# Optimization experiments

Measured on AMD Instinct MI355X. Metric: run time of the kernel, lower is better.

The kernel has to match this reference:

```python
import jax, jax.numpy as jnp
import numpy as np

VOCAB, D_MODEL, N_STATE, H_HEADS, LAYERS = 64, 512, 32, 16, 4
EXPAND = 2
D_INNER = EXPAND * D_MODEL          # 1024
P_HEAD = D_INNER // H_HEADS         # 64
CONV_DIM = D_INNER + 2 * N_STATE    # x, B, C share the depthwise conv
K_CONV = 4
D_IN_PROJ = 2 * D_INNER + 2 * N_STATE + H_HEADS  # z, x, B, C, dt
BATCH, SEQ = 4, 1024
EPS = 1e-5


def rmsnorm(x, w):
    return x * jax.lax.rsqrt(jnp.mean(x * x, axis=-1, keepdims=True) + EPS) * w


def silu(x):
    return x * jax.nn.sigmoid(x)


def causal_depthwise_conv(x, w, b):
    # x: [B,L,C], w: [C,K], b: [C]; causal (left) padding, depthwise groups
    xt = jnp.transpose(x, (0, 2, 1))  # [B,C,L]
    out = jax.lax.conv_general_dilated(xt, w[:, None, :], (1,), [(K_CONV - 1, 0)], feature_group_count=w.shape[0])
    return jnp.transpose(out, (0, 2, 1)) + b


def ssd(xh, dt, A, Bm, Cm, Dp):
    # Mamba2 SSD recurrence. xh [B,L,H,P], dt [B,L,H], A [H], Bm/Cm [B,L,N], Dp [H]
    dA = jnp.exp(dt * A)              # decay per (batch, step, head)
    dtx = dt[..., None] * xh          # [B,L,H,P]

    def step(h, inp):
        dA_t, dtx_t, B_t, C_t = inp
        # h: [B,H,P,N]
        h = dA_t[:, :, None, None] * h + dtx_t[..., None] * B_t[:, None, None, :]
        y = jnp.einsum('bhpn,bn->bhp', h, C_t)
        return h, y

    h0 = jnp.zeros((xh.shape[0], H_HEADS, P_HEAD, N_STATE), xh.dtype)
    _, ys = jax.lax.scan(step, h0, (jnp.moveaxis(dA, 1, 0), jnp.moveaxis(dtx, 1, 0), jnp.moveaxis(Bm, 1, 0), jnp.moveaxis(Cm, 1, 0)))
    return jnp.moveaxis(ys, 0, 1) + xh * Dp[None, None, :, None]


def mamba_block(x, norm_w, W_in, b_in, conv_w, conv_b, dt_bias, A_log, Dp, gnorm_w, W_out, b_out):
    res = x
    u = rmsnorm(x, norm_w)
    zxbcdt = u @ W_in + b_in                                # [B,L,D_IN_PROJ]
    z = zxbcdt[..., :D_INNER]
    xBC = zxbcdt[..., D_INNER:D_INNER + CONV_DIM]
    dt = zxbcdt[..., D_INNER + CONV_DIM:]                   # [B,L,H]
    xBC = silu(causal_depthwise_conv(xBC, conv_w, conv_b))
    xc = xBC[..., :D_INNER]
    Bm = xBC[..., D_INNER:D_INNER + N_STATE]
    Cm = xBC[..., D_INNER + N_STATE:]
    dt = jax.nn.softplus(dt + dt_bias)
    xh = xc.reshape(xc.shape[0], xc.shape[1], H_HEADS, P_HEAD)
    y = ssd(xh, dt, -jnp.exp(A_log), Bm, Cm, Dp)
    y = y.reshape(y.shape[0], y.shape[1], D_INNER)
    y = rmsnorm(y * silu(z), gnorm_w)                       # gated RMSNorm
    return res + y @ W_out + b_out


def forward(input_tokens, emb, norm_w, W_in, b_in, conv_w, conv_b, dt_bias, A_log, D_param, gnorm_w, W_out, b_out, head_w, head_b):
    h = emb[input_tokens]
    for i in range(LAYERS):
        h = mamba_block(h, norm_w[i], W_in[i], b_in[i], conv_w[i], conv_b[i], dt_bias[i], A_log[i], D_param[i], gnorm_w[i], W_out[i], b_out[i])
    return h @ head_w + head_b


def setup_inputs() -> dict:
    key = jax.random.key(0)
    ks = jax.random.split(key, 8)
    s = 0.02
    return {
        'input_tokens': jax.random.randint(ks[0], (BATCH, SEQ), 0, VOCAB),
        'emb': jax.random.normal(ks[1], (VOCAB, D_MODEL), jnp.float32) * s,
        'norm_w': jnp.ones((LAYERS, D_MODEL), jnp.float32),
        'W_in': jax.random.normal(ks[2], (LAYERS, D_MODEL, D_IN_PROJ), jnp.float32) * s,
        'b_in': jnp.zeros((LAYERS, D_IN_PROJ), jnp.float32),
        'conv_w': jax.random.normal(ks[3], (LAYERS, CONV_DIM, K_CONV), jnp.float32) * 0.1,
        'conv_b': jnp.zeros((LAYERS, CONV_DIM), jnp.float32),
        'dt_bias': jnp.tile(jnp.log(jnp.expm1(jnp.linspace(0.001, 0.1, H_HEADS, dtype=jnp.float32))), (LAYERS, 1)),
        'A_log': jnp.tile(jnp.log(jnp.arange(1, H_HEADS + 1, dtype=jnp.float32)), (LAYERS, 1)),
        'D_param': jnp.ones((LAYERS, H_HEADS), jnp.float32),
        'gnorm_w': jnp.ones((LAYERS, D_INNER), jnp.float32),
        'W_out': jax.random.normal(ks[4], (LAYERS, D_INNER, D_MODEL), jnp.float32) * s,
        'b_out': jnp.zeros((LAYERS, D_MODEL), jnp.float32),
        'head_w': jax.random.normal(ks[5], (D_MODEL, VOCAB), jnp.float32) * s,
        'head_b': jnp.zeros((VOCAB,), jnp.float32),
    }


def reference(input_tokens, emb, norm_w, W_in, b_in, conv_w, conv_b, dt_bias, A_log, D_param, gnorm_w, W_out, b_out, head_w, head_b):
    return forward(input_tokens, emb, norm_w, W_in, b_in, conv_w, conv_b, dt_bias, A_log, D_param, gnorm_w, W_out, b_out, head_w, head_b)
```

## Files before the change

### kernel.cpp

```cpp
#include <hip/hip_runtime.h>
#include <hip/hip_bf16.h>

#define VOCAB     64
#define D_MODEL   512
#define N_STATE   32
#define H_HEADS   16
#define LAYERS    4
#define D_INNER   1024
#define P_HEAD    64
#define CONV_DIM  1088
#define K_CONV    4
#define D_IN_PROJ 2128
#define NPAD_IN   2176
#define NPAD_HEAD 128
#define BATCH     4
#define SEQ       1024
#define NTOK      (BATCH*SEQ)
#define EPS       1e-5f
#define CL        64
#define NC        (SEQ/CL)
#define PSTR      80

typedef __bf16 bf16x8 __attribute__((ext_vector_type(8)));
typedef float  f32x4  __attribute__((ext_vector_type(4)));

__device__ __forceinline__ float sigmoidf_(float x) { return 1.f / (1.f + __expf(-x)); }
__device__ __forceinline__ float softplusf_(float x) { return (x > 20.f) ? x : log1pf(__expf(x)); }

__global__ void embed_kernel(const int* __restrict__ tok, const float* __restrict__ emb,
                             float* __restrict__ h) {
  int idx = blockIdx.x * 256 + threadIdx.x;
  if (idx >= NTOK * D_MODEL) return;
  int d = idx & (D_MODEL - 1);
  int t = idx >> 9;
  h[idx] = emb[tok[t] * D_MODEL + d];
}

__global__ void rmsnorm512_kernel(const float* __restrict__ x, const float* __restrict__ w,
                                  __bf16* __restrict__ out) {
  int tok = blockIdx.x;
  int tid = threadIdx.x;
  const float* xr = x + (size_t)tok * D_MODEL;
  float v0 = xr[tid], v1 = xr[tid + 256];
  float ss = v0 * v0 + v1 * v1;
  #pragma unroll
  for (int o = 32; o >= 1; o >>= 1) ss += __shfl_xor(ss, o);
  __shared__ float red[4];
  if ((tid & 63) == 0) red[tid >> 6] = ss;
  __syncthreads();
  float tot = red[0] + red[1] + red[2] + red[3];
  float sc = rsqrtf(tot * (1.f / D_MODEL) + EPS);
  out[(size_t)tok * D_MODEL + tid]       = (__bf16)(v0 * sc * w[tid]);
  out[(size_t)tok * D_MODEL + tid + 256] = (__bf16)(v1 * sc * w[tid + 256]);
}

__global__ void transpose_cast_kernel(const float* __restrict__ W, __bf16* __restrict__ Wt,
                                      int K, int N, int Npad) {
  W  += (size_t)blockIdx.z * K * N;
  Wt += (size_t)blockIdx.z * Npad * K;
  __shared__ float T[32][33];
  int n0 = blockIdx.x * 32, k0 = blockIdx.y * 32;
  int tx = threadIdx.x & 31, ty = threadIdx.x >> 5;
  #pragma unroll
  for (int i = 0; i < 4; i++) {
    int n = n0 + tx;
    T[ty + i * 8][tx] = (n < N) ? W[(size_t)(k0 + ty + i * 8) * N + n] : 0.f;
  }
  __syncthreads();
  #pragma unroll
  for (int i = 0; i < 4; i++)
    Wt[(size_t)(n0 + ty + i * 8) * K + k0 + tx] = (__bf16)T[tx][ty + i * 8];
}

#define TM 64
#define TN 128
#define TK 64
__global__ __launch_bounds__(256) void gemm_bf16_kernel(
    const __bf16* __restrict__ A, const __bf16* __restrict__ Bt,
    const float* __restrict__ bias, const float* __restrict__ res,
    float* __restrict__ C, __bf16* __restrict__ Cbf, int K, int N, int ldc) {
  __shared__ __bf16 As[TM * TK];
  __shared__ __bf16 Bs[TN * TK];
  int tid = threadIdx.x;
  int lane = tid & 63, wave = tid >> 6;
  int wm = wave >> 1, wn = wave & 1;
  int q = lane >> 4, l16 = lane & 15;
  size_t row0 = (size_t)blockIdx.y * TM;
  int col0 = blockIdx.x * TN;
  const __bf16* Ab = A + row0 * K;
  const __bf16* Bb = Bt + (size_t)col0 * K;

  bf16x8 pa[2], pb[4];
  #pragma unroll
  for (int r = 0; r < 2; r++) {
    int lin = r * 256 + tid;
    pa[r] = *(const bf16x8*)(Ab + (size_t)(lin >> 3) * K + (lin & 7) * 8);
  }
  #pragma unroll
  for (int r = 0; r < 4; r++) {
    int lin = r * 256 + tid;
    pb[r] = *(const bf16x8*)(Bb + (size_t)(lin >> 3) * K + (lin & 7) * 8);
  }

  f32x4 acc[2][4];
  #pragma unroll
  for (int i = 0; i < 2; i++)
    #pragma unroll
    for (int j = 0; j < 4; j++) acc[i][j] = (f32x4){0.f, 0.f, 0.f, 0.f};

  for (int k0 = 0; k0 < K; k0 += TK) {
    #pragma unroll
    for (int r = 0; r < 2; r++) { int lin = r * 256 + tid; *(bf16x8*)(As + lin * 8) = pa[r]; }
    #pragma unroll
    for (int r = 0; r < 4; r++) { int lin = r * 256 + tid; *(bf16x8*)(Bs + lin * 8) = pb[r]; }
    __syncthreads();
    int kn = k0 + TK;
    if (kn < K) {
      #pragma unroll
      for (int r = 0; r < 2; r++) {
        int lin = r * 256 + tid;
        pa[r] = *(const bf16x8*)(Ab + (size_t)(lin >> 3) * K + kn + (lin & 7) * 8);
      }
      #pragma unroll
      for (int r = 0; r < 4; r++) {
        int lin = r * 256 + tid;
        pb[r] = *(const bf16x8*)(Bb + (size_t)(lin >> 3) * K + kn + (lin & 7) * 8);
      }
    }
    #pragma unroll
    for (int ks = 0; ks < 2; ks++) {
      bf16x8 af[2], bfv[4];
      #pragma unroll
      for (int i = 0; i < 2; i++)
        af[i] = *(const bf16x8*)(As + (wm * 32 + i * 16 + l16) * TK + ks * 32 + q * 8);
      #pragma unroll
      for (int j = 0; j < 4; j++)
        bfv[j] = *(const bf16x8*)(Bs + (wn * 64 + j * 16 + l16) * TK + ks * 32 + q * 8);
      #pragma unroll
      for (int i = 0; i < 2; i++)
        #pragma unroll
        for (int j = 0; j < 4; j++)
          acc[i][j] = __builtin_amdgcn_mfma_f32_16x16x32_bf16(af[i], bfv[j], acc[i][j], 0, 0, 0);
    }
    __syncthreads();
  }

  #pragma unroll
  for (int i = 0; i < 2; i++) {
    size_t mrow = row0 + wm * 32 + i * 16 + q * 4;
    #pragma unroll
    for (int j = 0; j < 4; j++) {
      int col = col0 + wn * 64 + j * 16 + l16;
      if (col < N) {
        float bv = bias ? bias[col] : 0.f;
        #pragma unroll
        for (int rr = 0; rr < 4; rr++) {
          size_t off = (mrow + rr) * (size_t)ldc + col;
          float v = acc[i][j][rr] + bv;
          if (res) v += res[off];
          if (C)   C[off] = v;
          if (Cbf) Cbf[off] = (__bf16)v;
        }
      }
    }
  }
}

__device__ __forceinline__ void wave0_dt_cumsum(
    const __bf16* __restrict__ zxbf, const float* __restrict__ dt_bias,
    int b, int h, int t0, int tid, float* ldt, float* lcs) {
  if (tid < 64) {
    float dv = (float)zxbf[((size_t)(b * SEQ + t0 + tid)) * D_IN_PROJ + 2 * D_INNER + 2 * N_STATE + h]
               + dt_bias[h];
    float dtv = softplusf_(dv);
    float cs = dtv;
    #pragma unroll
    for (int off = 1; off < 64; off <<= 1) {
      float o = __shfl_up(cs, off);
      if (tid >= off) cs += o;
    }
    ldt[tid] = dtv;
    lcs[tid] = cs;
  }
}

__global__ __launch_bounds__(256) void ssd_local_kernel(
    const __bf16* __restrict__ zxbf, const float* __restrict__ conv_w,
    const float* __restrict__ conv_b, const float* __restrict__ dt_bias,
    const float* __restrict__ A_log,
    float* __restrict__ Slocal, float* __restrict__ dAprod) {
  int blk = blockIdx.x;
  int c = blk % NC;
  int h = (blk / NC) % H_HEADS;
  int b = blk / (NC * H_HEADS);
  int tid = threadIdx.x;
  int lane = tid & 63, wave = tid >> 6;
  int q = lane >> 4, l16 = lane & 15;
  int t0 = c * CL;
  float A = -__expf(A_log[h]);
  __shared__ __bf16 rawx[68][64];
  __shared__ __bf16 rawB[68][32];
  __shared__ __bf16 lxT[64][PSTR];
  __shared__ __bf16 lBT[32][PSTR];
  __shared__ float ldt[64], lcs[64];
  for (int i = tid; i < 68 * 8; i += 256) {
    int r = i >> 3, c0 = (i & 7) * 8;
    int gr = t0 - 3 + r;
    bf16x8 v;
    #pragma unroll
    for (int k = 0; k < 8; k++) v[k] = (__bf16)0.f;
    if (gr >= 0)
      v = *(const bf16x8*)(zxbf + ((size_t)(b * SEQ + gr)) * D_IN_PROJ + D_INNER + h * 64 + c0);
    *(bf16x8*)(&rawx[r][c0]) = v;
  }
  for (int i = tid; i < 68 * 4; i += 256) {
    int r = i >> 2, c0 = (i & 3) * 8;
    int gr = t0 - 3 + r;
    bf16x8 v;
    #pragma unroll
    for (int k = 0; k < 8; k++) v[k] = (__bf16)0.f;
    if (gr >= 0)
      v = *(const bf16x8*)(zxbf + ((size_t)(b * SEQ + gr)) * D_IN_PROJ + 2 * D_INNER + c0);
    *(bf16x8*)(&rawB[r][c0]) = v;
  }
  wave0_dt_cumsum(zxbf, dt_bias, b, h, t0, tid, ldt, lcs);
  __syncthreads();
  float cs63 = lcs[63];
  {
    int p = tid & 63;
    const float* w = conv_w + (h * 64 + p) * K_CONV;
    float w0 = w[0], w1 = w[1], w2 = w[2], w3 = w[3];
    float cb = conv_b[h * 64 + p];
    for (int i = tid; i < CL * 64; i += 256) {
      int t = i >> 6;
      float a = cb + w0 * (float)rawx[t][p] + w1 * (float)rawx[t + 1][p]
                   + w2 * (float)rawx[t + 2][p] + w3 * (float)rawx[t + 3][p];
      lxT[p][t] = (__bf16)(a * sigmoidf_(a));
    }
  }
  {
    int n = tid & 31;
    const float* w = conv_w + (D_INNER + n) * K_CONV;
    float w0 = w[0], w1 = w[1], w2 = w[2], w3 = w[3];
    float cb = conv_b[D_INNER + n];
    for (int i = tid; i < CL * 32; i += 256) {
      int t = i >> 5;
      float a = cb + w0 * (float)rawB[t][n] + w1 * (float)rawB[t + 1][n]
                   + w2 * (float)rawB[t + 2][n] + w3 * (float)rawB[t + 3][n];
      float v = a * sigmoidf_(a);
      float wt = ldt[t] * __expf(A * (cs63 - lcs[t]));
      lBT[n][t] = (__bf16)(v * wt);
    }
  }
  __syncthreads();
  f32x4 acc[2];
  acc[0] = (f32x4){0.f,0.f,0.f,0.f}; acc[1] = (f32x4){0.f,0.f,0.f,0.f};
  #pragma unroll
  for (int kb = 0; kb < 2; kb++) {
    bf16x8 af = *(const bf16x8*)(&lxT[wave * 16 + l16][kb * 32 + q * 8]);
    #pragma unroll
    for (int j = 0; j < 2; j++) {
      bf16x8 bf = *(const bf16x8*)(&lBT[l16 + 16 * j][kb * 32 + q * 8]);
      acc[j] = __builtin_amdgcn_mfma_f32_16x16x32_bf16(af, bf, acc[j], 0, 0, 0);
    }
  }
  float* dst = Slocal + (size_t)blk * 2048;
  #pragma unroll
  for (int j = 0; j < 2; j++) {
    int n = l16 + 16 * j;
    #pragma unroll
    for (int rr = 0; rr < 4; rr++) {
      int p = wave * 16 + q * 4 + rr;
      dst[p * 32 + n] = acc[j][rr];
    }
  }
  if (tid == 0) dAprod[blk] = __expf(A * cs63);
}

__global__ void ssd_combine_kernel(float* __restrict__ S, const float* __restrict__ dAprod) {
  int bh = blockIdx.x;
  int e = threadIdx.x * 8;
  float st[8] = {};
  for (int c = 0; c < NC; c++) {
    float* ptr = S + ((size_t)(bh * NC + c)) * 2048 + e;
    float pr = dAprod[bh * NC + c];
    float tmp[8];
    #pragma unroll
    for (int j = 0; j < 8; j++) tmp[j] = ptr[j];
    #pragma unroll
    for (int j = 0; j < 8; j++) { ptr[j] = st[j]; st[j] = pr * st[j] + tmp[j]; }
  }
}

__global__ __launch_bounds__(256) void ssd_out_kernel(
    const __bf16* __restrict__ zxbf, const float* __restrict__ conv_w,
    const float* __restrict__ conv_b, const float* __restrict__ dt_bias,
    const float* __restrict__ A_log, const float* __restrict__ Dp,
    const float* __restrict__ Sstart, __bf16* __restrict__ y) {
  int blk = blockIdx.x;
  int c = blk % NC;
  int h = (blk / NC) % H_HEADS;
  int b = blk / (NC * H_HEADS);
  int tid = threadIdx.x;
  int lane = tid & 63, wave = tid >> 6;
  int q = lane >> 4, l16 = lane & 15;
  int t0 = c * CL;
  float A = -__expf(A_log[h]);
  float D = Dp[h];
  __shared__ __bf16 rawbuf[2 * 68 * 64];
  __shared__ __bf16 lxT[64][PSTR];
  __shared__ __bf16 lB[64][32];
  __shared__ __bf16 lC[64][32];
  __shared__ __bf16 lS[64][32];
  __shared__ float ldt[64], lcs[64];
  __bf16* rawx = rawbuf;
  __bf16* rawBC = rawbuf + 68 * 64;
  for (int i = tid; i < 68 * 8; i += 256) {
    int r = i >> 3, c0 = (i & 7) * 8;
    int gr = t0 - 3 + r;
    bf16x8 vx, vbc;
    #pragma unroll
    for (int k = 0; k < 8; k++) { vx[k] = (__bf16)0.f; vbc[k] = (__bf16)0.f; }
    if (gr >= 0) {
      const __bf16* rowp = zxbf + ((size_t)(b * SEQ + gr)) * D_IN_PROJ;
      vx  = *(const bf16x8*)(rowp + D_INNER + h * 64 + c0);
      vbc = *(const bf16x8*)(rowp + 2 * D_INNER + c0);
    }
    *(bf16x8*)(rawx + r * 64 + c0)  = vx;
    *(bf16x8*)(rawBC + r * 64 + c0) = vbc;
  }
  wave0_dt_cumsum(zxbf, dt_bias, b, h, t0, tid, ldt, lcs);
  __syncthreads();
  {
    int p = tid & 63;
    const float* w = conv_w + (h * 64 + p) * K_CONV;
    float w0 = w[0], w1 = w[1], w2 = w[2], w3 = w[3];
    float cb = conv_b[h * 64 + p];
    for (int i = tid; i < CL * 64; i += 256) {
      int t = i >> 6;
      float a = cb + w0 * (float)rawx[t * 64 + p] + w1 * (float)rawx[(t + 1) * 64 + p]
                   + w2 * (float)rawx[(t + 2) * 64 + p] + w3 * (float)rawx[(t + 3) * 64 + p];
      lxT[p][t] = (__bf16)(a * sigmoidf_(a));
    }
  }
  {
    int col = tid & 63;
    const float* w = conv_w + (D_INNER + col) * K_CONV;
    float w0 = w[0], w1 = w[1], w2 = w[2], w3 = w[3];
    float cb = conv_b[D_INNER + col];
    for (int i = tid; i < CL * 64; i += 256) {
      int t = i >> 6;
      float a = cb + w0 * (float)rawBC[t * 64 + col] + w1 * (float)rawBC[(t + 1) * 64 + col]
                   + w2 * (float)rawBC[(t + 2) * 64 + col] + w3 * (float)rawBC[(t + 3) * 64 + col];
      float v = a * sigmoidf_(a);
      if (col < 32) lB[t][col] = (__bf16)v; else lC[t][col - 32] = (__bf16)v;
    }
  }
  {
    const float* src = Sstart + (size_t)blk * 2048;
    for (int i = tid; i < 2048; i += 256) lS[i >> 5][i & 31] = (__bf16)src[i];
  }
  __syncthreads();
  bf16x8 afC = *(const bf16x8*)(&lC[wave * 16 + l16][q * 8]);
  f32x4 accG[4], accI[4], accY[4];
  #pragma unroll
  for (int j = 0; j < 4; j++) {
    accG[j] = (f32x4){0.f,0.f,0.f,0.f};
    accI[j] = (f32x4){0.f,0.f,0.f,0.f};
    accY[j] = (f32x4){0.f,0.f,0.f,0.f};
  }
  #pragma unroll
  for (int j = 0; j < 4; j++) {
    bf16x8 bf = *(const bf16x8*)(&lB[l16 + 16 * j][q * 8]);
    accG[j] = __builtin_amdgcn_mfma_f32_16x16x32_bf16(afC, bf, accG[j], 0, 0, 0);
  }
  #pragma unroll
  for (int j = 0; j < 4; j++) {
    bf16x8 bf = *(const bf16x8*)(&lS[l16 + 16 * j][q * 8]);
    accI[j] = __builtin_amdgcn_mfma_f32_16x16x32_bf16(afC, bf, accI[j], 0, 0, 0);
  }
  __bf16* pP = rawbuf + wave * 16 * PSTR;
  #pragma unroll
  for (int j = 0; j < 4; j++) {
    int s = l16 + 16 * j;
    float css = lcs[s], dts = ldt[s];
    #pragma unroll
    for (int rr = 0; rr < 4; rr++) {
      int tl = q * 4 + rr;
      int t = wave * 16 + tl;
      float val = accG[j][rr] * __expf(A * (lcs[t] - css)) * dts;
      if (s == t) val += D;
      if (s > t) val = 0.f;
      pP[tl * PSTR + s] = (__bf16)val;
    }
  }
  #pragma unroll
  for (int kb = 0; kb < 2; kb++) {
    bf16x8 afP = *(const bf16x8*)(pP + l16 * PSTR + kb * 32 + q * 8);
    #pragma unroll
    for (int j = 0; j < 4; j++) {
      bf16x8 bf = *(const bf16x8*)(&lxT[l16 + 16 * j][kb * 32 + q * 8]);
      accY[j] = __builtin_amdgcn_mfma_f32_16x16x32_bf16(afP, bf, accY[j], 0, 0, 0);
    }
  }
  #pragma unroll
  for (int rr = 0; rr < 4; rr++) {
    int t = wave * 16 + q * 4 + rr;
    float cumt = __expf(A * lcs[t]);
    __bf16* yrow = y + ((size_t)(b * SEQ + t0 + t)) * D_INNER + h * 64;
    #pragma unroll
    for (int j = 0; j < 4; j++) {
      int p = l16 + 16 * j;
      yrow[p] = (__bf16)(accY[j][rr] + cumt * accI[j][rr]);
    }
  }
}

__global__ void gate_norm_kernel(const __bf16* __restrict__ zxbf, const float* __restrict__ gw,
                                 const __bf16* __restrict__ y, __bf16* __restrict__ ybf) {
  int tok = blockIdx.x;
  int tid = threadIdx.x;
  const __bf16* zr = zxbf + (size_t)tok * D_IN_PROJ;
  const __bf16* yr = y + (size_t)tok * D_INNER;
  float v[4];
  float ss = 0.f;
  #pragma unroll
  for (int i = 0; i < 4; i++) {
    int d = tid + i * 256;
    float z = (float)zr[d];
    float g = (float)yr[d] * z * sigmoidf_(z);
    v[i] = g;
    ss += g * g;
  }
  #pragma unroll
  for (int o = 32; o >= 1; o >>= 1) ss += __shfl_xor(ss, o);
  __shared__ float red[4];
  if ((tid & 63) == 0) red[tid >> 6] = ss;
  __syncthreads();
  float tot = red[0] + red[1] + red[2] + red[3];
  float sc = rsqrtf(tot * (1.f / D_INNER) + EPS);
  #pragma unroll
  for (int i = 0; i < 4; i++) {
    int d = tid + i * 256;
    ybf[(size_t)tok * D_INNER + d] = (__bf16)(v[i] * sc * gw[d]);
  }
}

extern "C" void kernel_launch(void* const* d_in, const int* in_sizes, int n_in,
                              void* d_out, int out_size, void* d_ws, size_t ws_size,
                              hipStream_t stream) {
  const int*   tok     = (const int*)  d_in[0];
  const float* emb     = (const float*)d_in[1];
  const float* norm_w  = (const float*)d_in[2];
  const float* W_in    = (const float*)d_in[3];
  const float* b_in    = (const float*)d_in[4];
  const float* conv_w  = (const float*)d_in[5];
  const float* conv_b  = (const float*)d_in[6];
  const float* dt_bias = (const float*)d_in[7];
  const float* A_log   = (const float*)d_in[8];
  const float* D_par   = (const float*)d_in[9];
  const float* gnorm_w = (const float*)d_in[10];
  const float* W_out   = (const float*)d_in[11];
  const float* b_out   = (const float*)d_in[12];
  const float* head_w  = (const float*)d_in[13];
  const float* head_b  = (const float*)d_in[14];
  float* out = (float*)d_out;

  char* p = (char*)d_ws;
  auto alloc = [&](size_t bytes) { void* r = (void*)p; p += (bytes + 255) & ~(size_t)255; return r; };
  float*  h      = (float*) alloc((size_t)NTOK * D_MODEL * 4);
  float*  slocal = (float*) alloc((size_t)BATCH * H_HEADS * NC * P_HEAD * N_STATE * 4);
  float*  daprod = (float*) alloc((size_t)BATCH * H_HEADS * NC * 4);
  __bf16* y      = (__bf16*)alloc((size_t)NTOK * D_INNER * 2);
  __bf16* zxbf   = (__bf16*)alloc((size_t)NTOK * D_IN_PROJ * 2);
  __bf16* ubf    = (__bf16*)alloc((size_t)NTOK * D_MODEL * 2);
  __bf16* ybf    = (__bf16*)alloc((size_t)NTOK * D_INNER * 2);
  __bf16* hbf    = (__bf16*)alloc((size_t)NTOK * D_MODEL * 2);
  __bf16* WtIn   = (__bf16*)alloc((size_t)LAYERS * NPAD_IN * D_MODEL * 2);
  __bf16* WtOut  = (__bf16*)alloc((size_t)LAYERS * D_MODEL * D_INNER * 2);
  __bf16* WtHead = (__bf16*)alloc((size_t)NPAD_HEAD * D_MODEL * 2);

  transpose_cast_kernel<<<dim3(NPAD_IN / 32, D_MODEL / 32, LAYERS), 256, 0, stream>>>(
      W_in, WtIn, D_MODEL, D_IN_PROJ, NPAD_IN);
  transpose_cast_kernel<<<dim3(D_MODEL / 32, D_INNER / 32, LAYERS), 256, 0, stream>>>(
      W_out, WtOut, D_INNER, D_MODEL, D_MODEL);
  transpose_cast_kernel<<<dim3(NPAD_HEAD / 32, D_MODEL / 32, 1), 256, 0, stream>>>(
      head_w, WtHead, D_MODEL, VOCAB, NPAD_HEAD);

  embed_kernel<<<(NTOK * D_MODEL + 255) / 256, 256, 0, stream>>>(tok, emb, h);

  for (int l = 0; l < LAYERS; l++) {
    rmsnorm512_kernel<<<NTOK, 256, 0, stream>>>(h, norm_w + (size_t)l * D_MODEL, ubf);

    gemm_bf16_kernel<<<dim3(NPAD_IN / TN, NTOK / TM), 256, 0, stream>>>(
        ubf, WtIn + (size_t)l * NPAD_IN * D_MODEL, b_in + (size_t)l * D_IN_PROJ,
        nullptr, nullptr, zxbf, D_MODEL, D_IN_PROJ, D_IN_PROJ);

    ssd_local_kernel<<<BATCH * H_HEADS * NC, 256, 0, stream>>>(
        zxbf, conv_w + (size_t)l * CONV_DIM * K_CONV, conv_b + (size_t)l * CONV_DIM,
        dt_bias + (size_t)l * H_HEADS, A_log + (size_t)l * H_HEADS, slocal, daprod);
    ssd_combine_kernel<<<BATCH * H_HEADS, 256, 0, stream>>>(slocal, daprod);
    ssd_out_kernel<<<BATCH * H_HEADS * NC, 256, 0, stream>>>(
        zxbf, conv_w + (size_t)l * CONV_DIM * K_CONV, conv_b + (size_t)l * CONV_DIM,
        dt_bias + (size_t)l * H_HEADS, A_log + (size_t)l * H_HEADS,
        D_par + (size_t)l * H_HEADS, slocal, y);

    gate_norm_kernel<<<NTOK, 256, 0, stream>>>(zxbf, gnorm_w + (size_t)l * D_INNER, y, ybf);

    gemm_bf16_kernel<<<dim3(D_MODEL / TN, NTOK / TM), 256, 0, stream>>>(
        ybf, WtOut + (size_t)l * D_MODEL * D_INNER, b_out + (size_t)l * D_MODEL, h, h,
        (l == LAYERS - 1) ? hbf : nullptr, D_INNER, D_MODEL, D_MODEL);
  }

  gemm_bf16_kernel<<<dim3(NPAD_HEAD / TN, NTOK / TM), 256, 0, stream>>>(
      hbf, WtHead, head_b, nullptr, out, nullptr, D_MODEL, VOCAB, VOCAB);
}
```

Before: 497.6 us.

## Add 128x128 register-prefetched GEMM for in-projection and parallelize chunk-state combine

Adds a dedicated GEMM kernel with 128x128 output tiles per block, 4x4 MFMA accumulators per wave and register prefetch of the next K-slice, used for the input projection. This raises operand reuse per LDS load and overlaps global loads with MFMA work. Separately, the chunk-state combine kernel now splits each (batch, head) across two blocks, caches the decay factors in shared memory, and loads all chunk states up front as float4 vectors before the serial scan. The larger tile roughly halves the grid and raises register pressure, which can lower occupancy.

```diff
diff --git a/kernel.cpp b/kernel.cpp
--- a/kernel.cpp
+++ b/kernel.cpp
@@ -161,6 +161,86 @@
           if (C)   C[off] = v;
           if (Cbf) Cbf[off] = (__bf16)v;
         }
+      }
+    }
+  }
+}
+
+__global__ __launch_bounds__(256) void gemm_bf16_128(
+    const __bf16* __restrict__ A, const __bf16* __restrict__ Bt,
+    const float* __restrict__ bias, __bf16* __restrict__ Cbf,
+    int K, int N, int ldc) {
+  __shared__ __bf16 As[128 * TK];
+  __shared__ __bf16 Bs[128 * TK];
+  int tid = threadIdx.x;
+  int lane = tid & 63, wave = tid >> 6;
+  int wm = wave >> 1, wn = wave & 1;
+  int q = lane >> 4, l16 = lane & 15;
+  size_t row0 = (size_t)blockIdx.y * 128;
+  int col0 = blockIdx.x * 128;
+  const __bf16* Ab = A + row0 * K;
+  const __bf16* Bb = Bt + (size_t)col0 * K;
+
+  bf16x8 pa[4], pb[4];
+  #pragma unroll
+  for (int r = 0; r < 4; r++) {
+    int lin = r * 256 + tid;
+    pa[r] = *(const bf16x8*)(Ab + (size_t)(lin >> 3) * K + (lin & 7) * 8);
+    pb[r] = *(const bf16x8*)(Bb + (size_t)(lin >> 3) * K + (lin & 7) * 8);
+  }
+
+  f32x4 acc[4][4];
+  #pragma unroll
+  for (int i = 0; i < 4; i++)
+    #pragma unroll
+    for (int j = 0; j < 4; j++) acc[i][j] = (f32x4){0.f, 0.f, 0.f, 0.f};
+
+  for (int k0 = 0; k0 < K; k0 += TK) {
+    #pragma unroll
+    for (int r = 0; r < 4; r++) {
+      int lin = r * 256 + tid;
+      *(bf16x8*)(As + lin * 8) = pa[r];
+      *(bf16x8*)(Bs + lin * 8) = pb[r];
+    }
+    __syncthreads();
+    int kn = k0 + TK;
+    if (kn < K) {
+      #pragma unroll
+      for (int r = 0; r < 4; r++) {
+        int lin = r * 256 + tid;
+        pa[r] = *(const bf16x8*)(Ab + (size_t)(lin >> 3) * K + kn + (lin & 7) * 8);
+        pb[r] = *(const bf16x8*)(Bb + (size_t)(lin >> 3) * K + kn + (lin & 7) * 8);
+      }
+    }
+    #pragma unroll
+    for (int ks = 0; ks < 2; ks++) {
+      bf16x8 af[4], bfv[4];
+      #pragma unroll
+      for (int i = 0; i < 4; i++)
+        af[i] = *(const bf16x8*)(As + (wm * 64 + i * 16 + l16) * TK + ks * 32 + q * 8);
+      #pragma unroll
+      for (int j = 0; j < 4; j++)
+        bfv[j] = *(const bf16x8*)(Bs + (wn * 64 + j * 16 + l16) * TK + ks * 32 + q * 8);
+      #pragma unroll
+      for (int i = 0; i < 4; i++)
+        #pragma unroll
+        for (int j = 0; j < 4; j++)
+          acc[i][j] = __builtin_amdgcn_mfma_f32_16x16x32_bf16(af[i], bfv[j], acc[i][j], 0, 0, 0);
+    }
+    __syncthreads();
+  }
+
+  #pragma unroll
+  for (int i = 0; i < 4; i++) {
+    size_t mrow = row0 + wm * 64 + i * 16 + q * 4;
+    #pragma unroll
+    for (int j = 0; j < 4; j++) {
+      int col = col0 + wn * 64 + j * 16 + l16;
+      if (col < N) {
+        float bv = bias[col];
+        #pragma unroll
+        for (int rr = 0; rr < 4; rr++)
+          Cbf[(mrow + rr) * (size_t)ldc + col] = (__bf16)(acc[i][j][rr] + bv);
       }
     }
   }
@@ -277,18 +357,23 @@
   if (tid == 0) dAprod[blk] = __expf(A * cs63);
 }
 
-__global__ void ssd_combine_kernel(float* __restrict__ S, const float* __restrict__ dAprod) {
-  int bh = blockIdx.x;
-  int e = threadIdx.x * 8;
-  float st[8] = {};
+__global__ __launch_bounds__(256) void ssd_combine_kernel(
+    float* __restrict__ S, const float* __restrict__ dAprod) {
+  int bh = blockIdx.x >> 1;
+  int half = blockIdx.x & 1;
+  __shared__ float pr[NC];
+  if (threadIdx.x < NC) pr[threadIdx.x] = dAprod[bh * NC + threadIdx.x];
+  __syncthreads();
+  float* base = S + (size_t)bh * NC * 2048 + half * 1024 + threadIdx.x * 4;
+  f32x4 tmp[NC];
+  #pragma unroll
+  for (int c = 0; c < NC; c++) tmp[c] = *(const f32x4*)(base + c * 2048);
+  f32x4 st = (f32x4){0.f, 0.f, 0.f, 0.f};
+  #pragma unroll
   for (int c = 0; c < NC; c++) {
-    float* ptr = S + ((size_t)(bh * NC + c)) * 2048 + e;
-    float pr = dAprod[bh * NC + c];
-    float tmp[8];
-    #pragma unroll
-    for (int j = 0; j < 8; j++) tmp[j] = ptr[j];
-    #pragma unroll
-    for (int j = 0; j < 8; j++) { ptr[j] = st[j]; st[j] = pr * st[j] + tmp[j]; }
+    f32x4 cur = tmp[c];
+    *(f32x4*)(base + c * 2048) = st;
+    st = pr[c] * st + cur;
   }
 }
 
@@ -492,14 +577,14 @@
   for (int l = 0; l < LAYERS; l++) {
     rmsnorm512_kernel<<<NTOK, 256, 0, stream>>>(h, norm_w + (size_t)l * D_MODEL, ubf);
 
-    gemm_bf16_kernel<<<dim3(NPAD_IN / TN, NTOK / TM), 256, 0, stream>>>(
+    gemm_bf16_128<<<dim3(NPAD_IN / 128, NTOK / 128), 256, 0, stream>>>(
         ubf, WtIn + (size_t)l * NPAD_IN * D_MODEL, b_in + (size_t)l * D_IN_PROJ,
-        nullptr, nullptr, zxbf, D_MODEL, D_IN_PROJ, D_IN_PROJ);
+        zxbf, D_MODEL, D_IN_PROJ, D_IN_PROJ);
 
     ssd_local_kernel<<<BATCH * H_HEADS * NC, 256, 0, stream>>>(
         zxbf, conv_w + (size_t)l * CONV_DIM * K_CONV, conv_b + (size_t)l * CONV_DIM,
         dt_bias + (size_t)l * H_HEADS, A_log + (size_t)l * H_HEADS, slocal, daprod);
-    ssd_combine_kernel<<<BATCH * H_HEADS, 256, 0, stream>>>(slocal, daprod);
+    ssd_combine_kernel<<<BATCH * H_HEADS * 2, 256, 0, stream>>>(slocal, daprod);
     ssd_out_kernel<<<BATCH * H_HEADS * NC, 256, 0, stream>>>(
         zxbf, conv_w + (size_t)l * CONV_DIM * K_CONV, conv_b + (size_t)l * CONV_DIM,
         dt_bias + (size_t)l * H_HEADS, A_log + (size_t)l * H_HEADS,
```

Result: no change. 497.7 us (+0.0%).
